# Performance work log

Hardware: AMD Instinct MI355X
Metric: run time of the kernel (lower is better)

The kernel has to match this reference:

```python
import jax, jax.numpy as jnp
import numpy as np

T = 96      # CONTEXT_SIZE
B = 32      # BATCH_SIZE
DIN = 256   # input_dim
H = 512     # hidden_dim
V = 128     # output_dim (vocab)


def setup_inputs() -> dict:
    key = jax.random.key(0)
    ks = jax.random.split(key, 16)
    s_in = 1.0 / np.sqrt(DIN)
    s_h = 1.0 / np.sqrt(H)

    def u(k, shape, s):
        return jax.random.uniform(k, shape, jnp.float32, -s, s)

    return {
        "x": jax.random.normal(ks[0], (B, T, DIN), jnp.float32),
        # input->hidden gate weights (no bias), one per timestep: [T, H, DIN]
        "Wif": u(ks[1], (T, H, DIN), s_in),
        "Wii": u(ks[2], (T, H, DIN), s_in),
        "Wic": u(ks[3], (T, H, DIN), s_in),
        "Wio": u(ks[4], (T, H, DIN), s_in),
        # hidden->hidden gate weights (+bias), one per timestep: [T, H, H], [T, H]
        "Whf_w": u(ks[5], (T, H, H), s_h), "Whf_b": u(ks[6], (T, H), s_h),
        "Whi_w": u(ks[7], (T, H, H), s_h), "Whi_b": u(ks[8], (T, H), s_h),
        "Whc_w": u(ks[9], (T, H, H), s_h), "Whc_b": u(ks[10], (T, H), s_h),
        "Who_w": u(ks[11], (T, H, H), s_h), "Who_b": u(ks[12], (T, H), s_h),
        # per-step output projections: [T, V, H], [T, V]
        "lin_w": u(ks[13], (T, V, H), s_h), "lin_b": u(ks[14], (T, V), s_h),
    }


def reference(x, Wif, Wii, Wic, Wio, Whf_w, Whf_b, Whi_w, Whi_b,
              Whc_w, Whc_b, Who_w, Who_b, lin_w, lin_b):
    sig = jax.nn.sigmoid

    # --- step 0: h_prev/c_prev are None -> hidden-path linears (and their
    # biases) are entirely absent, and c_t = i * c_bar (no forget term).
    x0 = x[:, 0]                                    # [B, DIN]
    i0 = sig(x0 @ Wii[0].T)
    cb0 = jnp.tanh(x0 @ Wic[0].T)
    o0 = sig(x0 @ Wio[0].T)
    c0 = i0 * cb0
    h0 = o0 * jnp.tanh(c0)                          # [B, H]
    logit0 = h0 @ lin_w[0].T + lin_b[0]             # [B, V]

    # --- steps 1..T-1: full gated update, distinct weights per step.
    def step(carry, ws):
        c, h = carry
        (xt, wif, whfw, whfb, wii, whiw, whib,
         wic, whcw, whcb, wio, whow, whob, lw, lb) = ws
        f = sig(xt @ wif.T + h @ whfw.T + whfb)
        i = sig(xt @ wii.T + h @ whiw.T + whib)
        cb = jnp.tanh(xt @ wic.T + h @ whcw.T + whcb)
        o = sig(xt @ wio.T + h @ whow.T + whob)
        c_t = f * c + i * cb
        h_t = o * jnp.tanh(c_t)
        return (c_t, h_t), h_t @ lw.T + lb

    xs = (jnp.swapaxes(x, 0, 1)[1:],               # [T-1, B, DIN]
          Wif[1:], Whf_w[1:], Whf_b[1:],
          Wii[1:], Whi_w[1:], Whi_b[1:],
          Wic[1:], Whc_w[1:], Whc_b[1:],
          Wio[1:], Who_w[1:], Who_b[1:],
          lin_w[1:], lin_b[1:])
    _, logits_rest = jax.lax.scan(step, (c0, h0), xs)   # [T-1, B, V]

    logits = jnp.concatenate([logit0[None], logits_rest], axis=0)  # [T, B, V]
    # original stacks [B, 1, V] per step along dim=1 -> [B, T, 1, V]
    return jnp.transpose(logits, (1, 0, 2))[:, :, None, :]
```

## Files before the change

kernel.cpp:

```cpp
#include <hip/hip_runtime.h>
#include <hip/hip_bf16.h>

#define TT 96
#define BB 32
#define DIN 256
#define HH 512
#define VV 128
#define NB 256

#define BAR() asm volatile("s_waitcnt lgkmcnt(0)\ns_barrier" ::: "memory")

__global__ __launch_bounds__(256) void phaseA_kernel(
    const float* __restrict__ x,
    const float* __restrict__ Wf, const float* __restrict__ Wi,
    const float* __restrict__ Wc, const float* __restrict__ Wo,
    float* __restrict__ Z)
{
    int bid  = blockIdx.x;
    int t    = bid >> 4;
    int tile = bid & 15;
    int g    = tile >> 2;
    int h0   = (tile & 3) * 128;
    const float* W = (g == 0) ? Wf : (g == 1) ? Wi : (g == 2) ? Wc : Wo;

    __shared__ float4 Xs4[32 * 64];
    __shared__ float4 Wc4[128 * 8];

    int tid = threadIdx.x;
    {
        int b   = tid >> 3;
        int kq8 = tid & 7;
        const float* src = x + ((size_t)b * TT + t) * DIN;
        int bx = b & 15;
        #pragma unroll
        for (int j = 0; j < 8; ++j) {
            int q = kq8 * 8 + j;
            Xs4[b * 64 + (q ^ bx)] = *reinterpret_cast<const float4*>(src + q * 4);
        }
    }

    int rg = tid >> 3;
    int bg = tid & 7;
    const float* wbase = W + ((size_t)t * HH + h0) * DIN;

    int srow[4], sgq[4];
    #pragma unroll
    for (int j = 0; j < 4; ++j) {
        int s = j * 256 + tid;
        srow[j] = s >> 3;
        sgq[j]  = (s & 7) ^ ((srow[j] >> 2) & 7);
    }

    float4 stg[4];
    #pragma unroll
    for (int j = 0; j < 4; ++j)
        stg[j] = *reinterpret_cast<const float4*>(wbase + (size_t)srow[j] * DIN + sgq[j] * 4);

    float acc[4][4];
    #pragma unroll
    for (int r = 0; r < 4; ++r)
        #pragma unroll
        for (int c = 0; c < 4; ++c) acc[r][c] = 0.f;

    for (int kc = 0; kc < 8; ++kc) {
        __syncthreads();
        #pragma unroll
        for (int j = 0; j < 4; ++j) Wc4[j * 256 + tid] = stg[j];
        __syncthreads();
        if (kc < 7) {
            #pragma unroll
            for (int j = 0; j < 4; ++j)
                stg[j] = *reinterpret_cast<const float4*>(
                    wbase + (size_t)srow[j] * DIN + (kc + 1) * 32 + sgq[j] * 4);
        }
        #pragma unroll
        for (int q = 0; q < 8; ++q) {
            float4 xv[4], wv[4];
            #pragma unroll
            for (int c = 0; c < 4; ++c) {
                int b = c * 8 + bg;
                xv[c] = Xs4[b * 64 + ((kc * 8 + q) ^ (b & 15))];
            }
            #pragma unroll
            for (int r = 0; r < 4; ++r)
                wv[r] = Wc4[(rg * 4 + r) * 8 + (q ^ (rg & 7))];
            #pragma unroll
            for (int r = 0; r < 4; ++r)
                #pragma unroll
                for (int c = 0; c < 4; ++c) {
                    acc[r][c] = fmaf(wv[r].x, xv[c].x, acc[r][c]);
                    acc[r][c] = fmaf(wv[r].y, xv[c].y, acc[r][c]);
                    acc[r][c] = fmaf(wv[r].z, xv[c].z, acc[r][c]);
                    acc[r][c] = fmaf(wv[r].w, xv[c].w, acc[r][c]);
                }
        }
    }

    size_t zbase = ((size_t)(t * 4 + g) * HH + h0 + rg * 4) * BB;
    #pragma unroll
    for (int r = 0; r < 4; ++r)
        #pragma unroll
        for (int c = 0; c < 4; ++c)
            Z[zbase + (size_t)r * BB + c * 8 + bg] = acc[r][c];
}

__global__ __launch_bounds__(512, 2) void lstm_persistent(
    const float* __restrict__ Whf, const float* __restrict__ Whi,
    const float* __restrict__ Whc, const float* __restrict__ Who,
    const float* __restrict__ bf,  const float* __restrict__ bi,
    const float* __restrict__ bc,  const float* __restrict__ bo,
    const float* __restrict__ Z,   float* __restrict__ Hall,
    unsigned* __restrict__ flags)
{
    int blk = blockIdx.x;
    int r0  = blk * 2;
    int tid = threadIdx.x;
    int ks  = tid >> 4;
    int bg  = tid & 15;

    __shared__ float pre[32][8][32];
    __shared__ float act[8][32];

    float creg = 0.f;

    for (int t = 0; t < TT; ++t) {
        float4 pfw[4];
        float4 pfz;
        float  pfb;
        bool pf_on = (t + 1 < TT) && (tid >= 256);
        int  idx   = tid - 256;
        if (pf_on) {
            #pragma unroll
            for (int j = 0; j < 4; ++j) {
                int f    = j * 256 + idx;
                int gate = f >> 8;
                int rl   = (f >> 7) & 1;
                int q    = f & 127;
                const float* wsrc = ((gate == 0) ? Whf : (gate == 1) ? Whi :
                                     (gate == 2) ? Whc : Who)
                                    + ((size_t)(t + 1) * HH + r0 + rl) * HH + q * 4;
                pfw[j] = *reinterpret_cast<const float4*>(wsrc);
            }
            if (idx < 64) {
                int g2 = idx >> 4, rl = (idx >> 3) & 1, qq = idx & 7;
                pfz = *reinterpret_cast<const float4*>(
                    Z + ((size_t)((t + 1) * 4 + g2) * HH + r0 + rl) * BB + qq * 4);
            }
            if (idx < 8) {
                int g2 = idx >> 1, rl = idx & 1;
                const float* bp = (g2 == 0) ? bf : (g2 == 1) ? bi : (g2 == 2) ? bc : bo;
                pfb = bp[(size_t)(t + 1) * HH + r0 + rl];
            }
        }

        float a[8][2];
        #pragma unroll
        for (int rg = 0; rg < 8; ++rg) { a[rg][0] = 0.f; a[rg][1] = 0.f; }

        if (t > 0) {
            int k0 = ks * 16;
            const float* hbase = Hall + (size_t)(t - 1) * HH * BB + (size_t)k0 * BB + 2 * bg;
            const float* wp[8];
            #pragma unroll
            for (int rl = 0; rl < 2; ++rl) {
                size_t wo = ((size_t)t * HH + r0 + rl) * HH + k0;
                wp[rl * 4 + 0] = Whf + wo;
                wp[rl * 4 + 1] = Whi + wo;
                wp[rl * 4 + 2] = Whc + wo;
                wp[rl * 4 + 3] = Who + wo;
            }
            #pragma unroll
            for (int q = 0; q < 4; ++q) {
                float2 hv[4];
                #pragma unroll
                for (int j = 0; j < 4; ++j)
                    hv[j] = *reinterpret_cast<const float2*>(hbase + (size_t)(q * 4 + j) * BB);
                #pragma unroll
                for (int rg = 0; rg < 8; ++rg) {
                    float4 w = *reinterpret_cast<const float4*>(wp[rg] + q * 4);
                    a[rg][0] = fmaf(w.x, hv[0].x, a[rg][0]); a[rg][1] = fmaf(w.x, hv[0].y, a[rg][1]);
                    a[rg][0] = fmaf(w.y, hv[1].x, a[rg][0]); a[rg][1] = fmaf(w.y, hv[1].y, a[rg][1]);
                    a[rg][0] = fmaf(w.z, hv[2].x, a[rg][0]); a[rg][1] = fmaf(w.z, hv[2].y, a[rg][1]);
                    a[rg][0] = fmaf(w.w, hv[3].x, a[rg][0]); a[rg][1] = fmaf(w.w, hv[3].y, a[rg][1]);
                }
            }
        }
        #pragma unroll
        for (int rg = 0; rg < 8; ++rg) {
            pre[ks][rg][2 * bg]     = a[rg][0];
            pre[ks][rg][2 * bg + 1] = a[rg][1];
        }

        BAR();

        if (tid < 256) {
            int rg2 = tid >> 5;
            int b   = tid & 31;
            int row = r0 + (rg2 >> 2);
            int g   = rg2 & 3;
            float s = 0.f;
            #pragma unroll
            for (int k2 = 0; k2 < 32; ++k2) s += pre[k2][rg2][b];
            s += Z[((size_t)(t * 4 + g) * HH + row) * BB + b];
            if (t > 0) {
                const float* bp = (g == 0) ? bf : (g == 1) ? bi : (g == 2) ? bc : bo;
                s += bp[t * HH + row];
            }
            act[rg2][b] = (g == 2) ? tanhf(s) : 1.f / (1.f + __expf(-s));
        }

        BAR();

        if (tid < 64) {
            int rl = tid >> 5, b = tid & 31;
            float cn = act[rl * 4 + 0][b] * creg + act[rl * 4 + 1][b] * act[rl * 4 + 2][b];
            creg = cn;
            float hn = act[rl * 4 + 3][b] * tanhf(cn);
            __hip_atomic_store(Hall + ((size_t)t * HH + r0 + rl) * BB + b, hn,
                               __ATOMIC_RELAXED, __HIP_MEMORY_SCOPE_AGENT);
            if (t + 1 < TT) {
                asm volatile("s_waitcnt vmcnt(0)" ::: "memory");
                if (tid == 0)
                    __hip_atomic_store(&flags[blk], (unsigned)(t + 1),
                                       __ATOMIC_RELAXED, __HIP_MEMORY_SCOPE_AGENT);
                {
                    const unsigned long long* f64 = (const unsigned long long*)flags;
                    unsigned long long tv = (unsigned long long)(unsigned)(t + 1);
                    tv |= tv << 32;
                    for (;;) {
                        unsigned long long v0 = __hip_atomic_load(
                            &f64[tid * 2], __ATOMIC_RELAXED, __HIP_MEMORY_SCOPE_AGENT);
                        unsigned long long v1 = __hip_atomic_load(
                            &f64[tid * 2 + 1], __ATOMIC_RELAXED, __HIP_MEMORY_SCOPE_AGENT);
                        if (__all(v0 == tv && v1 == tv)) break;
                        __builtin_amdgcn_s_sleep(1);
                    }
                }
            }
        } else if (pf_on) {
            float s = pfw[0].x + pfw[0].y + pfw[0].z + pfw[0].w
                    + pfw[1].x + pfw[1].y + pfw[1].z + pfw[1].w
                    + pfw[2].x + pfw[2].y + pfw[2].z + pfw[2].w
                    + pfw[3].x + pfw[3].y + pfw[3].z + pfw[3].w;
            if (idx < 64) s += pfz.x + pfz.y + pfz.z + pfz.w;
            if (idx < 8)  s += pfb;
            asm volatile("" :: "v"(s));
        }

        BAR();
    }
}

__global__ __launch_bounds__(256) void phaseC_kernel(
    const float* __restrict__ lw, const float* __restrict__ lb,
    const float* __restrict__ Hall, float* __restrict__ out)
{
    int t  = blockIdx.x >> 2;
    int v0 = (blockIdx.x & 3) << 5;
    int tid = threadIdx.x;
    int v  = v0 + (tid >> 3);
    int bg = tid & 7;
    const float* w  = lw + ((size_t)t * VV + v) * HH;
    const float* hp = Hall + (size_t)t * HH * BB;
    float acc0 = 0.f, acc1 = 0.f, acc2 = 0.f, acc3 = 0.f;
    #pragma unroll 4
    for (int k = 0; k < HH; ++k) {
        float wv = w[k];
        float4 hv = *reinterpret_cast<const float4*>(hp + (size_t)k * BB + bg * 4);
        acc0 = fmaf(wv, hv.x, acc0);
        acc1 = fmaf(wv, hv.y, acc1);
        acc2 = fmaf(wv, hv.z, acc2);
        acc3 = fmaf(wv, hv.w, acc3);
    }
    float bias = lb[t * VV + v];
    float r[4] = {acc0 + bias, acc1 + bias, acc2 + bias, acc3 + bias};
    #pragma unroll
    for (int j = 0; j < 4; ++j) {
        int b = bg * 4 + j;
        out[((size_t)b * TT + t) * VV + v] = r[j];
    }
}

extern "C" void kernel_launch(void* const* d_in, const int* in_sizes, int n_in,
                              void* d_out, int out_size, void* d_ws, size_t ws_size,
                              hipStream_t stream)
{
    const float* x     = (const float*)d_in[0];
    const float* Wif   = (const float*)d_in[1];
    const float* Wii   = (const float*)d_in[2];
    const float* Wic   = (const float*)d_in[3];
    const float* Wio   = (const float*)d_in[4];
    const float* Whf_w = (const float*)d_in[5];
    const float* Whf_b = (const float*)d_in[6];
    const float* Whi_w = (const float*)d_in[7];
    const float* Whi_b = (const float*)d_in[8];
    const float* Whc_w = (const float*)d_in[9];
    const float* Whc_b = (const float*)d_in[10];
    const float* Who_w = (const float*)d_in[11];
    const float* Who_b = (const float*)d_in[12];
    const float* lin_w = (const float*)d_in[13];
    const float* lin_b = (const float*)d_in[14];
    float* out = (float*)d_out;

    float*    Z     = (float*)d_ws;
    float*    Hall  = Z + (size_t)TT * 4 * HH * BB;
    unsigned* flags = (unsigned*)(Hall + (size_t)TT * HH * BB);

    hipMemsetAsync(flags, 0, NB * sizeof(unsigned), stream);

    phaseA_kernel<<<dim3(TT * 16), dim3(256), 0, stream>>>(x, Wif, Wii, Wic, Wio, Z);

    lstm_persistent<<<dim3(NB), dim3(512), 0, stream>>>(
        Whf_w, Whi_w, Whc_w, Who_w, Whf_b, Whi_b, Whc_b, Who_b, Z, Hall, flags);

    phaseC_kernel<<<dim3(TT * 4), dim3(256), 0, stream>>>(lin_w, lin_b, Hall, out);
}
```

Measured before the change: 1.024 ms.

## Decouple per-step grid barrier into distributed flag waits with double-buffered LDS

```diff
diff --git a/kernel.cpp b/kernel.cpp
--- a/kernel.cpp
+++ b/kernel.cpp
@@ -112,22 +112,24 @@
     const float* __restrict__ Z,   float* __restrict__ Hall,
     unsigned* __restrict__ flags)
 {
-    int blk = blockIdx.x;
-    int r0  = blk * 2;
-    int tid = threadIdx.x;
-    int ks  = tid >> 4;
-    int bg  = tid & 15;
-
-    __shared__ float pre[32][8][32];
-    __shared__ float act[8][32];
+    int blk  = blockIdx.x;
+    int r0   = blk * 2;
+    int tid  = threadIdx.x;
+    int ks   = tid >> 4;
+    int bg   = tid & 15;
+    int wid  = tid >> 6;
+    int lane = tid & 63;
+
+    __shared__ float pre[2][32][8][32];
 
     float creg = 0.f;
 
     for (int t = 0; t < TT; ++t) {
+        int p = t & 1;
+
         float4 pfw[4];
         float4 pfz;
-        float  pfb;
-        bool pf_on = (t + 1 < TT) && (tid >= 256);
+        bool pf_on = (t + 1 < TT) && (wid >= 4);
         int  idx   = tid - 256;
         if (pf_on) {
             #pragma unroll
@@ -146,18 +148,23 @@
                 pfz = *reinterpret_cast<const float4*>(
                     Z + ((size_t)((t + 1) * 4 + g2) * HH + r0 + rl) * BB + qq * 4);
             }
-            if (idx < 8) {
-                int g2 = idx >> 1, rl = idx & 1;
-                const float* bp = (g2 == 0) ? bf : (g2 == 1) ? bi : (g2 == 2) ? bc : bo;
-                pfb = bp[(size_t)(t + 1) * HH + r0 + rl];
-            }
-        }
-
-        float a[8][2];
-        #pragma unroll
-        for (int rg = 0; rg < 8; ++rg) { a[rg][0] = 0.f; a[rg][1] = 0.f; }
+        }
 
         if (t > 0) {
+            {
+                const unsigned* myf = flags + wid * 32 + (lane & 31);
+                for (;;) {
+                    unsigned v = __hip_atomic_load(myf, __ATOMIC_RELAXED,
+                                                   __HIP_MEMORY_SCOPE_AGENT);
+                    if (__all((int)(v >= (unsigned)t))) break;
+                    __builtin_amdgcn_s_sleep(1);
+                }
+            }
+
+            float a[8][2];
+            #pragma unroll
+            for (int rg = 0; rg < 8; ++rg) { a[rg][0] = 0.f; a[rg][1] = 0.f; }
+
             int k0 = ks * 16;
             const float* hbase = Hall + (size_t)(t - 1) * HH * BB + (size_t)k0 * BB + 2 * bg;
             const float* wp[8];
@@ -184,70 +191,62 @@
                     a[rg][0] = fmaf(w.w, hv[3].x, a[rg][0]); a[rg][1] = fmaf(w.w, hv[3].y, a[rg][1]);
                 }
             }
-        }
-        #pragma unroll
-        for (int rg = 0; rg < 8; ++rg) {
-            pre[ks][rg][2 * bg]     = a[rg][0];
-            pre[ks][rg][2 * bg + 1] = a[rg][1];
-        }
-
-        BAR();
-
-        if (tid < 256) {
-            int rg2 = tid >> 5;
-            int b   = tid & 31;
-            int row = r0 + (rg2 >> 2);
-            int g   = rg2 & 3;
-            float s = 0.f;
-            #pragma unroll
-            for (int k2 = 0; k2 < 32; ++k2) s += pre[k2][rg2][b];
-            s += Z[((size_t)(t * 4 + g) * HH + row) * BB + b];
-            if (t > 0) {
-                const float* bp = (g == 0) ? bf : (g == 1) ? bi : (g == 2) ? bc : bo;
-                s += bp[t * HH + row];
-            }
-            act[rg2][b] = (g == 2) ? tanhf(s) : 1.f / (1.f + __expf(-s));
-        }
-
-        BAR();
-
-        if (tid < 64) {
-            int rl = tid >> 5, b = tid & 31;
-            float cn = act[rl * 4 + 0][b] * creg + act[rl * 4 + 1][b] * act[rl * 4 + 2][b];
-            creg = cn;
-            float hn = act[rl * 4 + 3][b] * tanhf(cn);
-            __hip_atomic_store(Hall + ((size_t)t * HH + r0 + rl) * BB + b, hn,
-                               __ATOMIC_RELAXED, __HIP_MEMORY_SCOPE_AGENT);
-            if (t + 1 < TT) {
-                asm volatile("s_waitcnt vmcnt(0)" ::: "memory");
-                if (tid == 0)
-                    __hip_atomic_store(&flags[blk], (unsigned)(t + 1),
-                                       __ATOMIC_RELAXED, __HIP_MEMORY_SCOPE_AGENT);
-                {
-                    const unsigned long long* f64 = (const unsigned long long*)flags;
-                    unsigned long long tv = (unsigned long long)(unsigned)(t + 1);
-                    tv |= tv << 32;
-                    for (;;) {
-                        unsigned long long v0 = __hip_atomic_load(
-                            &f64[tid * 2], __ATOMIC_RELAXED, __HIP_MEMORY_SCOPE_AGENT);
-                        unsigned long long v1 = __hip_atomic_load(
-                            &f64[tid * 2 + 1], __ATOMIC_RELAXED, __HIP_MEMORY_SCOPE_AGENT);
-                        if (__all(v0 == tv && v1 == tv)) break;
-                        __builtin_amdgcn_s_sleep(1);
-                    }
-                }
-            }
-        } else if (pf_on) {
+            #pragma unroll
+            for (int rg = 0; rg < 8; ++rg) {
+                pre[p][ks][rg][2 * bg]     = a[rg][0];
+                pre[p][ks][rg][2 * bg + 1] = a[rg][1];
+            }
+        }
+
+        if (pf_on) {
             float s = pfw[0].x + pfw[0].y + pfw[0].z + pfw[0].w
                     + pfw[1].x + pfw[1].y + pfw[1].z + pfw[1].w
                     + pfw[2].x + pfw[2].y + pfw[2].z + pfw[2].w
                     + pfw[3].x + pfw[3].y + pfw[3].z + pfw[3].w;
             if (idx < 64) s += pfz.x + pfz.y + pfz.z + pfz.w;
-            if (idx < 8)  s += pfb;
             asm volatile("" :: "v"(s));
         }
 
         BAR();
+
+        if (wid == 0) {
+            int rl  = lane >> 5;
+            int b   = lane & 31;
+            int row = r0 + rl;
+            float s0 = 0.f, s1 = 0.f, s2 = 0.f, s3 = 0.f;
+            if (t > 0) {
+                #pragma unroll
+                for (int k2 = 0; k2 < 32; ++k2) {
+                    s0 += pre[p][k2][rl * 4 + 0][b];
+                    s1 += pre[p][k2][rl * 4 + 1][b];
+                    s2 += pre[p][k2][rl * 4 + 2][b];
+                    s3 += pre[p][k2][rl * 4 + 3][b];
+                }
+                s0 += bf[t * HH + row];
+                s1 += bi[t * HH + row];
+                s2 += bc[t * HH + row];
+                s3 += bo[t * HH + row];
+            }
+            s0 += Z[((size_t)(t * 4 + 0) * HH + row) * BB + b];
+            s1 += Z[((size_t)(t * 4 + 1) * HH + row) * BB + b];
+            s2 += Z[((size_t)(t * 4 + 2) * HH + row) * BB + b];
+            s3 += Z[((size_t)(t * 4 + 3) * HH + row) * BB + b];
+
+            float f  = 1.f / (1.f + __expf(-s0));
+            float i  = 1.f / (1.f + __expf(-s1));
+            float cb = tanhf(s2);
+            float o  = 1.f / (1.f + __expf(-s3));
+            float cn = f * creg + i * cb;
+            creg = cn;
+            float hn = o * tanhf(cn);
+
+            __hip_atomic_store(Hall + ((size_t)t * HH + row) * BB + b, hn,
+                               __ATOMIC_RELAXED, __HIP_MEMORY_SCOPE_AGENT);
+            asm volatile("s_waitcnt vmcnt(0)" ::: "memory");
+            if (lane == 0)
+                __hip_atomic_store(&flags[blk], (unsigned)(t + 1),
+                                   __ATOMIC_RELAXED, __HIP_MEMORY_SCOPE_AGENT);
+        }
     }
 }
 
```

After: 974.2 us. -4.9%, faster.
